# Kernel tuning notes

Hardware: AMD Instinct MI355X
Metric: run time of the kernel (lower is better)

Reference implementation:

```python
import jax, jax.numpy as jnp
import numpy as np

NUM_HEADS = 12


def setup_inputs() -> dict:
    key = jax.random.key(0)
    ks = jax.random.split(key, 6)
    B, N, C = 16, 576, 768
    H, D = NUM_HEADS, 768 // NUM_HEADS
    P = 16
    x = jax.random.normal(ks[0], (B, N, C), dtype=jnp.float32)
    prompt = jax.random.normal(ks[1], (B, 2, P, H, D), dtype=jnp.float32)
    act_scale = jax.random.uniform(ks[2], (2,), dtype=jnp.float32)
    qkv_w = jax.random.normal(ks[3], (3 * C, C), dtype=jnp.float32) * (C ** -0.5)
    proj_w = jax.random.normal(ks[4], (C, C), dtype=jnp.float32) * (C ** -0.5)
    proj_b = jnp.zeros((C,), dtype=jnp.float32)
    return {"x": x, "prompt": prompt, "act_scale": act_scale,
            "qkv_w": qkv_w, "proj_w": proj_w, "proj_b": proj_b}


def reference(x, prompt, act_scale, qkv_w, proj_w, proj_b):
    B, N, C = x.shape
    H = NUM_HEADS
    D = C // H
    scale = D ** -0.5
    # qkv projection: [B,N,3C] -> (3,B,H,N,D)
    qkv = (x @ qkv_w.T).reshape(B, N, 3, H, D).transpose(2, 0, 3, 1, 4)
    q, k, v = qkv[0], qkv[1], qkv[2]
    # prompt: [B,2,P,H,D] -> (2,B,H,P,D)
    pr = jnp.transpose(prompt, (1, 0, 3, 2, 4))
    key_prefix, value_prefix = pr[0], pr[1]        # [B,H,P,D]
    v = jnp.concatenate([value_prefix, v], axis=2)  # [B,H,P+N,D]
    # gated prefix scores
    prompt_attn = jnp.einsum('bhnd,bhpd->bhnp', q, key_prefix) * scale
    prompt_attn = prompt_attn + jnp.tanh(prompt_attn * act_scale[0]) * act_scale[1]
    # standard scores
    attn = jnp.einsum('bhnd,bhmd->bhnm', q, k) * scale
    attn = jnp.concatenate([prompt_attn, attn], axis=-1)  # [B,H,N,P+N]
    attn = jax.nn.softmax(attn, axis=-1)
    out = jnp.einsum('bhnm,bhmd->bhnd', attn, v)  # [B,H,N,D]
    out = out.transpose(0, 2, 1, 3).reshape(B, N, C)
    return out @ proj_w.T + proj_b
```

## Files before the change

kernel.cpp:

```cpp
#include <hip/hip_runtime.h>
#include <hip/hip_bf16.h>
#include <math.h>

namespace {

constexpr int kB = 16, kN = 576, kC = 768, kH = 12, kP = 16;
constexpr int kM = kB * kN;

typedef __attribute__((ext_vector_type(8))) __bf16 bf16x8;
typedef __attribute__((ext_vector_type(4))) float  f32x4;
typedef __attribute__((ext_vector_type(8))) unsigned short u16x8;

__device__ inline unsigned short f2bf(float f) {
  __bf16 h = (__bf16)f;
  return __builtin_bit_cast(unsigned short, h);
}
__device__ inline float bf2f(unsigned short u) {
  unsigned int x = ((unsigned int)u) << 16;
  return __builtin_bit_cast(float, x);
}
__device__ inline unsigned int pk2bf(float lo, float hi) {
  return (unsigned int)f2bf(lo) | ((unsigned int)f2bf(hi) << 16);
}
__device__ inline int xcd_swz(int hw, int nwg) {
  const int per = nwg >> 3;
  return (hw & 7) * per + (hw >> 3);
}

__global__ __launch_bounds__(256)
void cvt3(const float* __restrict__ x, const float* __restrict__ wq,
          const float* __restrict__ wp, unsigned short* __restrict__ xo,
          unsigned short* __restrict__ wqo, unsigned short* __restrict__ wpo) {
  const int bid = blockIdx.x;
  const float* in; unsigned short* out; int base;
  if (bid < 6912)       { in = x;  out = xo;  base = bid; }
  else if (bid < 8640)  { in = wq; out = wqo; base = bid - 6912; }
  else                  { in = wp; out = wpo; base = bid - 8640; }
  const int i = base * 256 + threadIdx.x;
  const float4 v = ((const float4*)in)[i];
  ((ushort4*)out)[i] = make_ushort4(f2bf(v.x), f2bf(v.y), f2bf(v.z), f2bf(v.w));
}

template<int OB>
__global__ __launch_bounds__(256)
void gemm_bf16(const unsigned short* __restrict__ A, const unsigned short* __restrict__ W,
               const float* __restrict__ bias, void* __restrict__ Yv, int Kd, int Nd) {
  __shared__ __align__(16) unsigned short As[2][4096];
  __shared__ __align__(16) unsigned short Bs[2][4096];
  const int tid  = threadIdx.x;
  const int wv   = tid >> 6, lane = tid & 63;
  const int gx   = Nd >> 7;
  const int lg   = xcd_swz(blockIdx.x, gridDim.x);
  const long bm  = (long)(lg / gx) * 128;
  const long bn  = (long)(lg % gx) * 128;
  const int wr   = (wv >> 1) * 64;
  const int wc   = (wv & 1) * 64;
  const int row15 = lane & 15, kg = lane >> 4;

  auto stage = [&](int buf, int kt) {
#pragma unroll
    for (int site = 0; site < 2; ++site) {
      const int p = site * 256 + tid;
      const unsigned short* srcA = A + (bm + (p >> 2)) * (long)Kd + kt + (p & 3) * 8;
      const unsigned short* srcB = W + (bn + (p >> 2)) * (long)Kd + kt + (p & 3) * 8;
      __builtin_amdgcn_global_load_lds(
          (const __attribute__((address_space(1))) unsigned int*)srcA,
          (__attribute__((address_space(3))) unsigned int*)(&As[buf][site * 2048 + wv * 512]),
          16, 0, 0);
      __builtin_amdgcn_global_load_lds(
          (const __attribute__((address_space(1))) unsigned int*)srcB,
          (__attribute__((address_space(3))) unsigned int*)(&Bs[buf][site * 2048 + wv * 512]),
          16, 0, 0);
    }
  };

  f32x4 acc[4][4] = {};
  stage(0, 0);
  __syncthreads();

  const int nt = Kd >> 5;
  for (int t = 0; t < nt; ++t) {
    const int cur = t & 1;
    if (t + 1 < nt) stage(cur ^ 1, (t + 1) << 5);

    bf16x8 af[4], bf_[4];
#pragma unroll
    for (int mi = 0; mi < 4; ++mi)
      af[mi] = *(const bf16x8*)(&As[cur][(wr + mi * 16 + row15) * 32 + kg * 8]);
#pragma unroll
    for (int ni = 0; ni < 4; ++ni)
      bf_[ni] = *(const bf16x8*)(&Bs[cur][(wc + ni * 16 + row15) * 32 + kg * 8]);
#pragma unroll
    for (int mi = 0; mi < 4; ++mi)
#pragma unroll
      for (int ni = 0; ni < 4; ++ni)
        acc[mi][ni] = __builtin_amdgcn_mfma_f32_16x16x32_bf16(af[mi], bf_[ni], acc[mi][ni], 0, 0, 0);
    __syncthreads();
  }

  const int r4 = kg * 4;
#pragma unroll
  for (int ni = 0; ni < 4; ++ni) {
    const long col = bn + wc + ni * 16 + row15;
    if constexpr (OB) {
      unsigned short* Y = (unsigned short*)Yv;
#pragma unroll
      for (int mi = 0; mi < 4; ++mi)
#pragma unroll
        for (int j = 0; j < 4; ++j)
          Y[(bm + wr + mi * 16 + r4 + j) * (long)Nd + col] = f2bf(acc[mi][ni][j]);
    } else {
      float* Y = (float*)Yv;
      const float bv = bias ? bias[col] : 0.0f;
#pragma unroll
      for (int mi = 0; mi < 4; ++mi)
#pragma unroll
        for (int j = 0; j < 4; ++j)
          Y[(bm + wr + mi * 16 + r4 + j) * (long)Nd + col] = acc[mi][ni][j] + bv;
    }
  }
}

__global__ __launch_bounds__(256)
void attn_mfma(const unsigned short* __restrict__ qkv, const float* __restrict__ prompt,
               const float* __restrict__ act_scale, unsigned short* __restrict__ attn_out) {
  const int lg = xcd_swz(blockIdx.x, gridDim.x);
  const int qt = lg % 9, bh = lg / 9;
  const int h = bh % kH, b = bh / kH;
  const int tid = threadIdx.x, wv = tid >> 6, lane = tid & 63;
  const int q15 = lane & 15, kg = lane >> 4;

  __shared__ __align__(16) unsigned short Klds[2][2048];
  __shared__ __align__(16) unsigned short Vt[2][2560];
  __shared__ __align__(16) unsigned short Plds[4][640];

  const float a0 = act_scale[0], a1 = act_scale[1];
  const int vkp = tid & 15;
  const int vdg = tid >> 4;
  const int kr  = wv * 8 + (lane >> 3), ksl = lane & 7;

  bf16x8 qf[2];
  {
    const unsigned short* qrow = qkv + (size_t)(b * kN + qt * 64 + wv * 16 + q15) * 2304 + h * 64;
#pragma unroll
    for (int dh = 0; dh < 2; ++dh) {
      u16x8 raw = *(const u16x8*)(qrow + dh * 32 + kg * 8);
      u16x8 sc;
#pragma unroll
      for (int j = 0; j < 8; ++j) sc[j] = f2bf(bf2f(raw[j]) * 0.125f);
      qf[dh] = __builtin_bit_cast(bf16x8, sc);
    }
  }

  if (tid < 128) {
    const int r = tid >> 3, s = tid & 7;
    const float* src = prompt + (((size_t)(b * 2) * kP + r) * kH + h) * 64 + s * 8;
    const float4 f0 = *(const float4*)src, f1 = *(const float4*)(src + 4);
    *(uint4*)(&Klds[0][r * 64 + ((s ^ (r & 7)) << 3)]) =
        make_uint4(pk2bf(f0.x, f0.y), pk2bf(f0.z, f0.w), pk2bf(f1.x, f1.y), pk2bf(f1.z, f1.w));
  }
  {
    unsigned int w0 = 0, w1 = 0, w2 = 0, w3 = 0;
    if (vkp < 8) {
      const float* s0 = prompt + (((size_t)(b * 2 + 1) * kP + 2 * vkp) * kH + h) * 64 + vdg * 4;
      const float* s1 = s0 + kH * 64;
      const float4 x0 = *(const float4*)s0;
      const float4 y0 = *(const float4*)s1;
      w0 = pk2bf(x0.x, y0.x);
      w1 = pk2bf(x0.y, y0.y);
      w2 = pk2bf(x0.z, y0.z);
      w3 = pk2bf(x0.w, y0.w);
    }
    unsigned short* vdst = &Vt[0][vdg * 160 + 2 * vkp];
    *(unsigned int*)(vdst)        = w0;
    *(unsigned int*)(vdst + 40)   = w1;
    *(unsigned int*)(vdst + 80)   = w2;
    *(unsigned int*)(vdst + 120)  = w3;
  }
  __syncthreads();

  f32x4 o[4] = {};
  float mrun = -3.0e38f, lrun = 0.0f;

  for (int ch = 0; ch < 19; ++ch) {
    const int cur = ch & 1;

    if (ch < 18) {
      const int nk = ch * 32 + kr;
      const unsigned short* src = qkv + (size_t)(b * kN + nk) * 2304 + 768 + h * 64 + ((ksl ^ (kr & 7)) << 3);
      __builtin_amdgcn_global_load_lds(
          (const __attribute__((address_space(1))) unsigned int*)src,
          (__attribute__((address_space(3))) unsigned int*)(&Klds[cur ^ 1][wv * 512]), 16, 0, 0);

      const int nv = ch * 32 + 2 * vkp;
      const unsigned short* s0 = qkv + (size_t)(b * kN + nv) * 2304 + 1536 + h * 64 + vdg * 4;
      const ushort4 v0 = *(const ushort4*)s0;
      const ushort4 v1 = *(const ushort4*)(s0 + 2304);
      unsigned short* vdst = &Vt[cur ^ 1][vdg * 160 + 2 * vkp];
      *(unsigned int*)(vdst)       = (unsigned int)v0.x | ((unsigned int)v1.x << 16);
      *(unsigned int*)(vdst + 40)  = (unsigned int)v0.y | ((unsigned int)v1.y << 16);
      *(unsigned int*)(vdst + 80)  = (unsigned int)v0.z | ((unsigned int)v1.z << 16);
      *(unsigned int*)(vdst + 120) = (unsigned int)v0.w | ((unsigned int)v1.w << 16);
    }

    f32x4 c0 = {}, c1;
    {
      const unsigned short* krow = &Klds[cur][q15 * 64];
      const bf16x8 k00 = *(const bf16x8*)(krow + ((kg ^ (q15 & 7)) << 3));
      const bf16x8 k01 = *(const bf16x8*)(krow + (((4 + kg) ^ (q15 & 7)) << 3));
      c0 = __builtin_amdgcn_mfma_f32_16x16x32_bf16(k00, qf[0], c0, 0, 0, 0);
      c0 = __builtin_amdgcn_mfma_f32_16x16x32_bf16(k01, qf[1], c0, 0, 0, 0);
    }
    if (ch != 0) {
      const unsigned short* krow = &Klds[cur][(q15 + 16) * 64];
      const bf16x8 k10 = *(const bf16x8*)(krow + ((kg ^ (q15 & 7)) << 3));
      const bf16x8 k11 = *(const bf16x8*)(krow + (((4 + kg) ^ (q15 & 7)) << 3));
      f32x4 t = {};
      t  = __builtin_amdgcn_mfma_f32_16x16x32_bf16(k10, qf[0], t, 0, 0, 0);
      c1 = __builtin_amdgcn_mfma_f32_16x16x32_bf16(k11, qf[1], t, 0, 0, 0);
    } else {
      c1[0] = c1[1] = c1[2] = c1[3] = -1.0e30f;
#pragma unroll
      for (int j = 0; j < 4; ++j) {
        const float s = c0[j];
        const float e = __expf(2.0f * s * a0);
        c0[j] = s + ((e - 1.0f) / (e + 1.0f)) * a1;
      }
    }

    float cmax = fmaxf(fmaxf(fmaxf(c0[0], c0[1]), fmaxf(c0[2], c0[3])),
                       fmaxf(fmaxf(c1[0], c1[1]), fmaxf(c1[2], c1[3])));
    cmax = fmaxf(cmax, __shfl_xor(cmax, 16, 64));
    cmax = fmaxf(cmax, __shfl_xor(cmax, 32, 64));
    if (!__all(cmax - mrun <= 8.0f)) {
      const float mnew = fmaxf(mrun, cmax);
      const float resc = __expf(mrun - mnew);
      lrun *= resc;
      float rq[4];
#pragma unroll
      for (int jr = 0; jr < 4; ++jr) rq[jr] = __shfl(resc, kg * 4 + jr, 64);
#pragma unroll
      for (int nb = 0; nb < 4; ++nb)
#pragma unroll
        for (int jr = 0; jr < 4; ++jr) o[nb][jr] *= rq[jr];
      mrun = mnew;
    }
    float pe[8];
#pragma unroll
    for (int j = 0; j < 4; ++j) { pe[j] = __expf(c0[j] - mrun); pe[4 + j] = __expf(c1[j] - mrun); }
    float psum = ((pe[0] + pe[1]) + (pe[2] + pe[3])) + ((pe[4] + pe[5]) + (pe[6] + pe[7]));
    psum += __shfl_xor(psum, 16, 64);
    psum += __shfl_xor(psum, 32, 64);
    lrun += psum;

    unsigned short* pl = &Plds[wv][q15 * 40];
    *(uint2*)(pl + 4 * kg)      = make_uint2(pk2bf(pe[0], pe[1]), pk2bf(pe[2], pe[3]));
    *(uint2*)(pl + 16 + 4 * kg) = make_uint2(pk2bf(pe[4], pe[5]), pk2bf(pe[6], pe[7]));

    const bf16x8 pa = *(const bf16x8*)(&Plds[wv][q15 * 40 + kg * 8]);
#pragma unroll
    for (int nb = 0; nb < 4; ++nb) {
      const bf16x8 bv = *(const bf16x8*)(&Vt[cur][(nb * 16 + q15) * 40 + kg * 8]);
      o[nb] = __builtin_amdgcn_mfma_f32_16x16x32_bf16(pa, bv, o[nb], 0, 0, 0);
    }

    __syncthreads();
  }

  const float inv = 1.0f / lrun;
  float iq[4];
#pragma unroll
  for (int jr = 0; jr < 4; ++jr) iq[jr] = __shfl(inv, kg * 4 + jr, 64);
  unsigned short* obase = attn_out + (size_t)(b * kN + qt * 64 + wv * 16) * 768 + h * 64;
#pragma unroll
  for (int nb = 0; nb < 4; ++nb)
#pragma unroll
    for (int jr = 0; jr < 4; ++jr)
      obase[(size_t)(kg * 4 + jr) * 768 + nb * 16 + q15] = f2bf(o[nb][jr] * iq[jr]);
}

}

extern "C" void kernel_launch(void* const* d_in, const int* in_sizes, int n_in,
                              void* d_out, int out_size, void* d_ws, size_t ws_size,
                              hipStream_t stream) {
  const float* x         = (const float*)d_in[0];
  const float* prompt    = (const float*)d_in[1];
  const float* act_scale = (const float*)d_in[2];
  const float* qkv_w     = (const float*)d_in[3];
  const float* proj_w    = (const float*)d_in[4];
  const float* proj_b    = (const float*)d_in[5];
  float* out = (float*)d_out;

  char* ws = (char*)d_ws;
  unsigned short* qkvb   = (unsigned short*)ws;
  unsigned short* xa     = (unsigned short*)(ws + 42467328);
  unsigned short* qkvwb  = (unsigned short*)(ws + 42467328 + 14155776);
  unsigned short* projwb = (unsigned short*)(ws + 42467328 + 14155776 + 3538944);

  cvt3<<<9216, 256, 0, stream>>>(x, qkv_w, proj_w, xa, qkvwb, projwb);

  gemm_bf16<1><<<(3 * kC / 128) * (kM / 128), 256, 0, stream>>>(xa, qkvwb, nullptr, qkvb, kC, 3 * kC);
  attn_mfma<<<(kN / 64) * kH * kB, 256, 0, stream>>>(qkvb, prompt, act_scale, xa);
  gemm_bf16<0><<<(kC / 128) * (kM / 128), 256, 0, stream>>>(xa, projwb, proj_b, out, kC, kC);
}
```

Measured before the change: 137.4 us.

## Enlarge attention tiles to 96 queries and 64-key chunks with specialized loader waves

```diff
diff --git a/kernel.cpp b/kernel.cpp
--- a/kernel.cpp
+++ b/kernel.cpp
@@ -121,27 +121,27 @@
   }
 }
 
-__global__ __launch_bounds__(256)
+__global__ __launch_bounds__(384, 4)
 void attn_mfma(const unsigned short* __restrict__ qkv, const float* __restrict__ prompt,
                const float* __restrict__ act_scale, unsigned short* __restrict__ attn_out) {
   const int lg = xcd_swz(blockIdx.x, gridDim.x);
-  const int qt = lg % 9, bh = lg / 9;
+  const int qt = lg % 6, bh = lg / 6;
   const int h = bh % kH, b = bh / kH;
   const int tid = threadIdx.x, wv = tid >> 6, lane = tid & 63;
   const int q15 = lane & 15, kg = lane >> 4;
 
-  __shared__ __align__(16) unsigned short Klds[2][2048];
-  __shared__ __align__(16) unsigned short Vt[2][2560];
-  __shared__ __align__(16) unsigned short Plds[4][640];
+  __shared__ __align__(16) unsigned short Klds[2][4096];
+  __shared__ __align__(16) unsigned short Vt[2][4096];
+  __shared__ __align__(16) unsigned short Plds[6][1024];
 
   const float a0 = act_scale[0], a1 = act_scale[1];
-  const int vkp = tid & 15;
-  const int vdg = tid >> 4;
-  const int kr  = wv * 8 + (lane >> 3), ksl = lane & 7;
+  const int sw  = q15 & 7;
+  const int sl0 = (kg ^ sw) << 3;
+  const int sl1 = ((4 + kg) ^ sw) << 3;
 
   bf16x8 qf[2];
   {
-    const unsigned short* qrow = qkv + (size_t)(b * kN + qt * 64 + wv * 16 + q15) * 2304 + h * 64;
+    const unsigned short* qrow = qkv + (size_t)(b * kN + qt * 96 + wv * 16 + q15) * 2304 + h * 64;
 #pragma unroll
     for (int dh = 0; dh < 2; ++dh) {
       u16x8 raw = *(const u16x8*)(qrow + dh * 32 + kg * 8);
@@ -159,77 +159,87 @@
     *(uint4*)(&Klds[0][r * 64 + ((s ^ (r & 7)) << 3)]) =
         make_uint4(pk2bf(f0.x, f0.y), pk2bf(f0.z, f0.w), pk2bf(f1.x, f1.y), pk2bf(f1.z, f1.w));
   }
-  {
-    unsigned int w0 = 0, w1 = 0, w2 = 0, w3 = 0;
+  if (tid < 256) {
+    const int vkp = tid & 15, vdg = tid >> 4;
+    unsigned int w[4] = {0, 0, 0, 0};
     if (vkp < 8) {
       const float* s0 = prompt + (((size_t)(b * 2 + 1) * kP + 2 * vkp) * kH + h) * 64 + vdg * 4;
       const float* s1 = s0 + kH * 64;
       const float4 x0 = *(const float4*)s0;
       const float4 y0 = *(const float4*)s1;
-      w0 = pk2bf(x0.x, y0.x);
-      w1 = pk2bf(x0.y, y0.y);
-      w2 = pk2bf(x0.z, y0.z);
-      w3 = pk2bf(x0.w, y0.w);
-    }
-    unsigned short* vdst = &Vt[0][vdg * 160 + 2 * vkp];
-    *(unsigned int*)(vdst)        = w0;
-    *(unsigned int*)(vdst + 40)   = w1;
-    *(unsigned int*)(vdst + 80)   = w2;
-    *(unsigned int*)(vdst + 120)  = w3;
+      w[0] = pk2bf(x0.x, y0.x); w[1] = pk2bf(x0.y, y0.y);
+      w[2] = pk2bf(x0.z, y0.z); w[3] = pk2bf(x0.w, y0.w);
+    }
+#pragma unroll
+    for (int j = 0; j < 4; ++j) {
+      const int d = vdg * 4 + j;
+      Plds[0][0] += 0;
+      *(unsigned int*)(&Vt[0][d * 64 + (((vkp >> 2) ^ (d & 7)) << 3) + (vkp & 3) * 2]) = w[j];
+    }
   }
   __syncthreads();
 
   f32x4 o[4] = {};
   float mrun = -3.0e38f, lrun = 0.0f;
 
-  for (int ch = 0; ch < 19; ++ch) {
+  const int vkp = tid & 31;
+  const int vdg = (tid >> 5) & 7;
+
+  for (int ch = 0; ch < 10; ++ch) {
     const int cur = ch & 1;
 
-    if (ch < 18) {
-      const int nk = ch * 32 + kr;
-      const unsigned short* src = qkv + (size_t)(b * kN + nk) * 2304 + 768 + h * 64 + ((ksl ^ (kr & 7)) << 3);
-      __builtin_amdgcn_global_load_lds(
-          (const __attribute__((address_space(1))) unsigned int*)src,
-          (__attribute__((address_space(3))) unsigned int*)(&Klds[cur ^ 1][wv * 512]), 16, 0, 0);
-
-      const int nv = ch * 32 + 2 * vkp;
-      const unsigned short* s0 = qkv + (size_t)(b * kN + nv) * 2304 + 1536 + h * 64 + vdg * 4;
-      const ushort4 v0 = *(const ushort4*)s0;
-      const ushort4 v1 = *(const ushort4*)(s0 + 2304);
-      unsigned short* vdst = &Vt[cur ^ 1][vdg * 160 + 2 * vkp];
-      *(unsigned int*)(vdst)       = (unsigned int)v0.x | ((unsigned int)v1.x << 16);
-      *(unsigned int*)(vdst + 40)  = (unsigned int)v0.y | ((unsigned int)v1.y << 16);
-      *(unsigned int*)(vdst + 80)  = (unsigned int)v0.z | ((unsigned int)v1.z << 16);
-      *(unsigned int*)(vdst + 120) = (unsigned int)v0.w | ((unsigned int)v1.w << 16);
-    }
-
-    f32x4 c0 = {}, c1;
-    {
-      const unsigned short* krow = &Klds[cur][q15 * 64];
-      const bf16x8 k00 = *(const bf16x8*)(krow + ((kg ^ (q15 & 7)) << 3));
-      const bf16x8 k01 = *(const bf16x8*)(krow + (((4 + kg) ^ (q15 & 7)) << 3));
-      c0 = __builtin_amdgcn_mfma_f32_16x16x32_bf16(k00, qf[0], c0, 0, 0, 0);
-      c0 = __builtin_amdgcn_mfma_f32_16x16x32_bf16(k01, qf[1], c0, 0, 0, 0);
-    }
-    if (ch != 0) {
-      const unsigned short* krow = &Klds[cur][(q15 + 16) * 64];
-      const bf16x8 k10 = *(const bf16x8*)(krow + ((kg ^ (q15 & 7)) << 3));
-      const bf16x8 k11 = *(const bf16x8*)(krow + (((4 + kg) ^ (q15 & 7)) << 3));
-      f32x4 t = {};
-      t  = __builtin_amdgcn_mfma_f32_16x16x32_bf16(k10, qf[0], t, 0, 0, 0);
-      c1 = __builtin_amdgcn_mfma_f32_16x16x32_bf16(k11, qf[1], t, 0, 0, 0);
-    } else {
-      c1[0] = c1[1] = c1[2] = c1[3] = -1.0e30f;
+    u16x8 vld0, vld1;
+    const bool doV = (ch < 9) && (wv < 4);
+    if (ch < 9) {
+      if (doV) {
+        const int nv = ch * 64 + 2 * vkp;
+        const unsigned short* s0 = qkv + (size_t)(b * kN + nv) * 2304 + 1536 + h * 64 + vdg * 8;
+        vld0 = *(const u16x8*)s0;
+        vld1 = *(const u16x8*)(s0 + 2304);
+      } else if (wv >= 4) {
+        const int rbase = (wv - 4) * 32;
+#pragma unroll
+        for (int g = 0; g < 4; ++g) {
+          const int r = rbase + g * 8 + (lane >> 3), s = lane & 7;
+          const unsigned short* src =
+              qkv + (size_t)(b * kN + ch * 64 + r) * 2304 + 768 + h * 64 + ((s ^ (r & 7)) << 3);
+          __builtin_amdgcn_global_load_lds(
+              (const __attribute__((address_space(1))) unsigned int*)src,
+              (__attribute__((address_space(3))) unsigned int*)(&Klds[cur ^ 1][(rbase + g * 8) * 64]),
+              16, 0, 0);
+        }
+      }
+    }
+
+    f32x4 c[4];
+    const int nkb = (ch == 0) ? 1 : 4;
+#pragma unroll
+    for (int kb = 0; kb < 4; ++kb) {
+      if (kb < nkb) {
+        const unsigned short* krow = &Klds[cur][(kb * 16 + q15) * 64];
+        const bf16x8 k0 = *(const bf16x8*)(krow + sl0);
+        const bf16x8 k1 = *(const bf16x8*)(krow + sl1);
+        f32x4 t = {};
+        t = __builtin_amdgcn_mfma_f32_16x16x32_bf16(k0, qf[0], t, 0, 0, 0);
+        c[kb] = __builtin_amdgcn_mfma_f32_16x16x32_bf16(k1, qf[1], t, 0, 0, 0);
+      } else {
+        c[kb][0] = c[kb][1] = c[kb][2] = c[kb][3] = -1.0e30f;
+      }
+    }
+    if (ch == 0) {
 #pragma unroll
       for (int j = 0; j < 4; ++j) {
-        const float s = c0[j];
+        const float s = c[0][j];
         const float e = __expf(2.0f * s * a0);
-        c0[j] = s + ((e - 1.0f) / (e + 1.0f)) * a1;
-      }
-    }
-
-    float cmax = fmaxf(fmaxf(fmaxf(c0[0], c0[1]), fmaxf(c0[2], c0[3])),
-                       fmaxf(fmaxf(c1[0], c1[1]), fmaxf(c1[2], c1[3])));
+        c[0][j] = s + ((e - 1.0f) / (e + 1.0f)) * a1;
+      }
+    }
+
+    float cmax = -3.0e38f;
+#pragma unroll
+    for (int kb = 0; kb < 4; ++kb)
+#pragma unroll
+      for (int j = 0; j < 4; ++j) cmax = fmaxf(cmax, c[kb][j]);
     cmax = fmaxf(cmax, __shfl_xor(cmax, 16, 64));
     cmax = fmaxf(cmax, __shfl_xor(cmax, 32, 64));
     if (!__all(cmax - mrun <= 8.0f)) {
@@ -245,23 +255,46 @@
         for (int jr = 0; jr < 4; ++jr) o[nb][jr] *= rq[jr];
       mrun = mnew;
     }
-    float pe[8];
-#pragma unroll
-    for (int j = 0; j < 4; ++j) { pe[j] = __expf(c0[j] - mrun); pe[4 + j] = __expf(c1[j] - mrun); }
-    float psum = ((pe[0] + pe[1]) + (pe[2] + pe[3])) + ((pe[4] + pe[5]) + (pe[6] + pe[7]));
+    float pe[16];
+    float psum = 0.0f;
+#pragma unroll
+    for (int kb = 0; kb < 4; ++kb)
+#pragma unroll
+      for (int j = 0; j < 4; ++j) { pe[kb * 4 + j] = __expf(c[kb][j] - mrun); psum += pe[kb * 4 + j]; }
     psum += __shfl_xor(psum, 16, 64);
     psum += __shfl_xor(psum, 32, 64);
     lrun += psum;
 
-    unsigned short* pl = &Plds[wv][q15 * 40];
-    *(uint2*)(pl + 4 * kg)      = make_uint2(pk2bf(pe[0], pe[1]), pk2bf(pe[2], pe[3]));
-    *(uint2*)(pl + 16 + 4 * kg) = make_uint2(pk2bf(pe[4], pe[5]), pk2bf(pe[6], pe[7]));
-
-    const bf16x8 pa = *(const bf16x8*)(&Plds[wv][q15 * 40 + kg * 8]);
+    {
+      unsigned short* pl = &Plds[wv][q15 * 64];
+#pragma unroll
+      for (int kb = 0; kb < 4; ++kb) {
+        const int off = (((kb * 2 + (kg >> 1)) ^ sw) << 3) + (kg & 1) * 4;
+        *(uint2*)(pl + off) = make_uint2(pk2bf(pe[kb * 4], pe[kb * 4 + 1]),
+                                         pk2bf(pe[kb * 4 + 2], pe[kb * 4 + 3]));
+      }
+    }
+    if (doV) {
+#pragma unroll
+      for (int j = 0; j < 8; ++j) {
+        const int d = vdg * 8 + j;
+        *(unsigned int*)(&Vt[cur ^ 1][d * 64 + (((vkp >> 2) ^ (d & 7)) << 3) + (vkp & 3) * 2]) =
+            (unsigned int)vld0[j] | ((unsigned int)vld1[j] << 16);
+      }
+    }
+
+    const unsigned short* pw = &Plds[wv][q15 * 64];
+    const bf16x8 pa0 = *(const bf16x8*)(pw + sl0);
+    const bf16x8 pa1 = *(const bf16x8*)(pw + sl1);
 #pragma unroll
     for (int nb = 0; nb < 4; ++nb) {
-      const bf16x8 bv = *(const bf16x8*)(&Vt[cur][(nb * 16 + q15) * 40 + kg * 8]);
-      o[nb] = __builtin_amdgcn_mfma_f32_16x16x32_bf16(pa, bv, o[nb], 0, 0, 0);
+      const unsigned short* vr = &Vt[cur][(nb * 16 + q15) * 64];
+      const bf16x8 bv0 = *(const bf16x8*)(vr + sl0);
+      o[nb] = __builtin_amdgcn_mfma_f32_16x16x32_bf16(pa0, bv0, o[nb], 0, 0, 0);
+      if (ch != 0) {
+        const bf16x8 bv1 = *(const bf16x8*)(vr + sl1);
+        o[nb] = __builtin_amdgcn_mfma_f32_16x16x32_bf16(pa1, bv1, o[nb], 0, 0, 0);
+      }
     }
 
     __syncthreads();
@@ -271,7 +304,7 @@
   float iq[4];
 #pragma unroll
   for (int jr = 0; jr < 4; ++jr) iq[jr] = __shfl(inv, kg * 4 + jr, 64);
-  unsigned short* obase = attn_out + (size_t)(b * kN + qt * 64 + wv * 16) * 768 + h * 64;
+  unsigned short* obase = attn_out + (size_t)(b * kN + qt * 96 + wv * 16) * 768 + h * 64;
 #pragma unroll
   for (int nb = 0; nb < 4; ++nb)
 #pragma unroll
@@ -301,6 +334,6 @@
   cvt3<<<9216, 256, 0, stream>>>(x, qkv_w, proj_w, xa, qkvwb, projwb);
 
   gemm_bf16<1><<<(3 * kC / 128) * (kM / 128), 256, 0, stream>>>(xa, qkvwb, nullptr, qkvb, kC, 3 * kC);
-  attn_mfma<<<(kN / 64) * kH * kB, 256, 0, stream>>>(qkvb, prompt, act_scale, xa);
+  attn_mfma<<<(kN / 96) * kH * kB, 384, 0, stream>>>(qkvb, prompt, act_scale, xa);
   gemm_bf16<0><<<(kC / 128) * (kM / 128), 256, 0, stream>>>(xa, projwb, proj_b, out, kC, kC);
 }
```

Result: no change. 136.4 us (-0.7%).
